# Kernel tuning notes

Hardware: AMD Instinct MI355X
Metric: run time of the kernel (lower is better)

## Reference

```python
import jax, jax.numpy as jnp
import numpy as np

B, S, H = 2, 1024, 1024
N_IN, N_PROC = 512, 32


def _l2norm(x, eps=1e-12):
    n = jnp.linalg.norm(x, axis=-1, keepdims=True)
    return x / jnp.maximum(n, eps)


def setup_inputs() -> dict:
    key = jax.random.key(0)
    k1, k2, k3, k4 = jax.random.split(key, 4)
    intermediate = jax.random.normal(k1, (B, S, H), dtype=jnp.float32)
    input_activations = jax.random.normal(k2, (B, S, N_IN), dtype=jnp.float32)
    # params (torch defaults: pattern_templates ~ randn; Linear weight ~ U scaled)
    pattern_templates = jax.random.normal(k3, (N_PROC, N_IN), dtype=jnp.float32)
    bound = 1.0 / np.sqrt(H)
    W_transform = jax.random.uniform(k4, (N_PROC * H, H), dtype=jnp.float32,
                                     minval=-bound, maxval=bound)
    return {"intermediate": intermediate, "input_activations": input_activations,
            "pattern_templates": pattern_templates, "W_transform": W_transform}


def reference(intermediate, input_activations, pattern_templates, W_transform):
    # pattern matching -> soft routing weights  [B,S,N_proc]
    act_norm = _l2norm(input_activations)
    tmpl_norm = _l2norm(pattern_templates)
    process_activations = jax.nn.sigmoid(
        jnp.einsum('bsi,ni->bsn', act_norm, tmpl_norm))
    # dispatch: weighted sum over sequence (batched GEMM instead of bcast-mul-sum)
    contexts = jnp.einsum('bsh,bsn->bnh', intermediate, process_activations)
    norm = process_activations.sum(axis=1)[..., None] + 1e-8  # [B,N_proc,1]
    contexts = contexts / norm
    # per-process-neuron HxH transform (torch Linear weight is [out,in])
    Wn = W_transform.reshape(N_PROC, H, H)  # [n, k(out), h(in)]
    transformed = jnp.einsum('bnh,nkh->bnk', contexts, Wn)
    # combine back to tokens  [B,S,H]
    combined = jnp.einsum('bnh,bsn->bsh', transformed, process_activations)
    return combined, process_activations
```

## Files before the change

kernel.cpp:

```cpp
#include <hip/hip_runtime.h>
#include <math.h>

#define B 2
#define S 1024
#define H 1024
#define NIN 512
#define NP 32
#define SC 16
#define SCHUNK (S / SC)

__global__ void k_pattern(const float* __restrict__ act, const float* __restrict__ tmpl,
                          float* __restrict__ P, float* __restrict__ nrm) {
    __shared__ float act_lds[8][NIN];
    __shared__ float invn[NP];
    __shared__ float psum[8][NP];
    int tid = threadIdx.x;
    int t0 = blockIdx.x * 8;
    int b  = t0 >> 10;

    {
        int n = tid >> 3, sub = tid & 7;
        const float* tr = tmpl + (size_t)n * NIN;
        float ss = 0.f;
#pragma unroll 16
        for (int k = 0; k < 64; ++k) { float x = tr[sub + 8 * k]; ss += x * x; }
        ss += __shfl_xor(ss, 1);
        ss += __shfl_xor(ss, 2);
        ss += __shfl_xor(ss, 4);
        if (sub == 0) invn[n] = 1.f / fmaxf(sqrtf(ss), 1e-12f);
    }
    {
        const float* src = act + (size_t)t0 * NIN;
        float* dst = &act_lds[0][0];
        for (int k = tid; k < 8 * NIN; k += 256) dst[k] = src[k];
    }
    __syncthreads();

    int tok = tid >> 5;
    int n   = tid & 31;
    float ss = 0.f;
#pragma unroll
    for (int k = 0; k < 16; ++k) { float x = act_lds[tok][n + 32 * k]; ss += x * x; }
#pragma unroll
    for (int m = 16; m; m >>= 1) ss += __shfl_xor(ss, m);
    float inva = 1.f / fmaxf(sqrtf(ss), 1e-12f);

    const float4* t4 = (const float4*)(tmpl + (size_t)n * NIN);
    const float4* a4 = (const float4*)(&act_lds[tok][0]);
    float d = 0.f;
#pragma unroll 8
    for (int i = 0; i < NIN / 4; ++i) {
        float4 tv = t4[i];
        float4 av = a4[i];
        d += tv.x * av.x + tv.y * av.y + tv.z * av.z + tv.w * av.w;
    }
    d *= inva * invn[n];
    float p = 1.f / (1.f + expf(-d));
    P[(size_t)(t0 + tok) * NP + n] = p;

    psum[tok][n] = p;
    __syncthreads();
    if (tid < NP) {
        float s = 0.f;
#pragma unroll
        for (int t = 0; t < 8; ++t) s += psum[t][tid];
        unsafeAtomicAdd(&nrm[b * NP + tid], s);
    }
}

__global__ void k_ctx(const float* __restrict__ I, const float* __restrict__ P,
                      float* __restrict__ ctx) {
    int bid = blockIdx.x;
    int ht = bid & 7;
    int sc = (bid >> 3) & (SC - 1);
    int b  = bid >> 7;
    int tid = threadIdx.x;
    __shared__ float Pl[SCHUNK][NP];
    int s0 = sc * SCHUNK;
    {
        const float* src = P + ((size_t)b * S + s0) * NP;
        float* dst = &Pl[0][0];
        for (int k = tid; k < SCHUNK * NP; k += 256) dst[k] = src[k];
    }
    __syncthreads();
    int hl = tid & 127;
    int g  = tid >> 7;
    int h  = ht * 128 + hl;
    float acc[16];
#pragma unroll
    for (int j = 0; j < 16; ++j) acc[j] = 0.f;
    const float* Ip = I + ((size_t)b * S + s0) * H + h;
    for (int s = 0; s < SCHUNK; ++s) {
        float x = Ip[(size_t)s * H];
#pragma unroll
        for (int j = 0; j < 16; ++j) acc[j] += x * Pl[s][g * 16 + j];
    }
#pragma unroll
    for (int j = 0; j < 16; ++j)
        unsafeAtomicAdd(&ctx[((size_t)b * NP + g * 16 + j) * H + h], acc[j]);
}

__global__ __launch_bounds__(256, 4)
void k_transform(const float* __restrict__ W, const float* __restrict__ ctx,
                 const float* __restrict__ nrm, float* __restrict__ T) {
    int bid = blockIdx.x;
    int n  = bid >> 6;
    int rg = bid & 63;
    int tid = threadIdx.x;
    int w = tid >> 6, lane = tid & 63;

    float inv0 = 1.f / (nrm[n] + 1e-8f);
    float inv1 = 1.f / (nrm[NP + n] + 1e-8f);

    const float4* c0g = (const float4*)(ctx + (size_t)n * H);
    const float4* c1g = (const float4*)(ctx + ((size_t)NP + n) * H);
    float4 c0[4], c1[4];
#pragma unroll
    for (int it = 0; it < 4; ++it) {
        float4 v = c0g[it * 64 + lane];
        c0[it] = make_float4(v.x * inv0, v.y * inv0, v.z * inv0, v.w * inv0);
        float4 u = c1g[it * 64 + lane];
        c1[it] = make_float4(u.x * inv1, u.y * inv1, u.z * inv1, u.w * inv1);
    }

    int row0 = rg * 16 + w * 4;
    const float4* Wr = (const float4*)(W + ((size_t)n * H + row0) * H);
    float a0[4] = {0.f, 0.f, 0.f, 0.f};
    float a1[4] = {0.f, 0.f, 0.f, 0.f};
#pragma unroll
    for (int it = 0; it < 4; ++it) {
#pragma unroll
        for (int r = 0; r < 4; ++r) {
            float4 wv = Wr[r * 256 + it * 64 + lane];
            a0[r] += wv.x * c0[it].x + wv.y * c0[it].y + wv.z * c0[it].z + wv.w * c0[it].w;
            a1[r] += wv.x * c1[it].x + wv.y * c1[it].y + wv.z * c1[it].z + wv.w * c1[it].w;
        }
    }
#pragma unroll
    for (int r = 0; r < 4; ++r) {
#pragma unroll
        for (int off = 32; off; off >>= 1) {
            a0[r] += __shfl_xor(a0[r], off);
            a1[r] += __shfl_xor(a1[r], off);
        }
    }
    if (lane == 0) {
#pragma unroll
        for (int r = 0; r < 4; ++r) {
            T[(size_t)n * H + row0 + r] = a0[r];
            T[((size_t)NP + n) * H + row0 + r] = a1[r];
        }
    }
}

__global__ void k_combine(const float* __restrict__ T, const float* __restrict__ P,
                          float* __restrict__ out) {
    int bid = blockIdx.x;
    int ht = bid & 3;
    int sc = (bid >> 2) & 63;
    int b  = bid >> 8;
    int tid = threadIdx.x;
    __shared__ float Tl[NP][256];
    __shared__ float Pl[16][NP];
    int h0 = ht * 256;
    for (int k = tid; k < NP * 256; k += 256) {
        int n = k >> 8, h = k & 255;
        Tl[n][h] = T[((size_t)b * NP + n) * H + h0 + h];
    }
    int s0 = sc * 16;
    {
        const float* src = P + ((size_t)b * S + s0) * NP;
        float* dst = &Pl[0][0];
        for (int k = tid; k < 16 * NP; k += 256) dst[k] = src[k];
    }
    __syncthreads();
    for (int s = 0; s < 16; ++s) {
        float acc = 0.f;
#pragma unroll
        for (int n = 0; n < NP; ++n) acc += Pl[s][n] * Tl[n][tid];
        out[((size_t)b * S + s0 + s) * H + h0 + tid] = acc;
    }
}

extern "C" void kernel_launch(void* const* d_in, const int* in_sizes, int n_in,
                              void* d_out, int out_size, void* d_ws, size_t ws_size,
                              hipStream_t stream) {
    const float* I    = (const float*)d_in[0];
    const float* act  = (const float*)d_in[1];
    const float* tmpl = (const float*)d_in[2];
    const float* W    = (const float*)d_in[3];
    float* out  = (float*)d_out;
    float* Pout = out + (size_t)B * S * H;

    float* ws  = (float*)d_ws;
    float* ctx = ws;
    float* nrm = ctx + (size_t)B * NP * H;
    float* T   = nrm + B * NP;

    hipMemsetAsync(ctx, 0, (size_t)(B * NP * H + B * NP) * sizeof(float), stream);
    k_pattern  <<<B * S / 8,              256, 0, stream>>>(act, tmpl, Pout, nrm);
    k_ctx      <<<B * SC * 8,             256, 0, stream>>>(I, Pout, ctx);
    k_transform<<<NP * 64,                256, 0, stream>>>(W, ctx, nrm, T);
    k_combine  <<<B * (S/16) * (H/256),   256, 0, stream>>>(T, Pout, out);
}
```

Measured before the change: 78.91 us.

## Restructure pattern dot, replace ctx atomics with partial+reduce, register-block combine

k_pattern now has each lane compute partial dots against all 32 templates over a slice of the activation, then reduces them with wave shuffles, so template reads are spread across lanes instead of each lane streaming one template row. k_ctx writes per-chunk partial sums to workspace, and a new reduce kernel sums them, which removes the float atomics and most of the memset at the cost of an extra launch and extra global traffic. k_combine keeps 16 output rows in registers and reads P directly from global memory instead of staging it in LDS. P is also read directly in ctx instead of through LDS.

```diff
diff --git a/kernel.cpp b/kernel.cpp
--- a/kernel.cpp
+++ b/kernel.cpp
@@ -9,8 +9,9 @@
 #define SC 16
 #define SCHUNK (S / SC)
 
-__global__ void k_pattern(const float* __restrict__ act, const float* __restrict__ tmpl,
-                          float* __restrict__ P, float* __restrict__ nrm) {
+__global__ __launch_bounds__(256)
+void k_pattern(const float* __restrict__ act, const float* __restrict__ tmpl,
+               float* __restrict__ P, float* __restrict__ nrm) {
     __shared__ float act_lds[8][NIN];
     __shared__ float invn[NP];
     __shared__ float psum[8][NP];
@@ -19,46 +20,58 @@
     int b  = t0 >> 10;
 
     {
-        int n = tid >> 3, sub = tid & 7;
+        const float4* src = (const float4*)(act + (size_t)t0 * NIN);
+        float4* dst = (float4*)(&act_lds[0][0]);
+        for (int k = tid; k < 8 * NIN / 4; k += 256) dst[k] = src[k];
+    }
+    {
+        int n = tid >> 3, s8 = tid & 7;
         const float* tr = tmpl + (size_t)n * NIN;
         float ss = 0.f;
 #pragma unroll 16
-        for (int k = 0; k < 64; ++k) { float x = tr[sub + 8 * k]; ss += x * x; }
-        ss += __shfl_xor(ss, 1);
-        ss += __shfl_xor(ss, 2);
-        ss += __shfl_xor(ss, 4);
-        if (sub == 0) invn[n] = 1.f / fmaxf(sqrtf(ss), 1e-12f);
-    }
-    {
-        const float* src = act + (size_t)t0 * NIN;
-        float* dst = &act_lds[0][0];
-        for (int k = tid; k < 8 * NIN; k += 256) dst[k] = src[k];
+        for (int k = 0; k < 64; ++k) { float x = tr[s8 + 8 * k]; ss += x * x; }
+        ss += __shfl_xor(ss, 1); ss += __shfl_xor(ss, 2); ss += __shfl_xor(ss, 4);
+        if (s8 == 0) invn[n] = 1.f / fmaxf(sqrtf(ss), 1e-12f);
     }
     __syncthreads();
 
     int tok = tid >> 5;
-    int n   = tid & 31;
+    int sub = tid & 31;
     float ss = 0.f;
 #pragma unroll
-    for (int k = 0; k < 16; ++k) { float x = act_lds[tok][n + 32 * k]; ss += x * x; }
+    for (int k = 0; k < 16; ++k) { float x = act_lds[tok][sub + 32 * k]; ss += x * x; }
 #pragma unroll
     for (int m = 16; m; m >>= 1) ss += __shfl_xor(ss, m);
     float inva = 1.f / fmaxf(sqrtf(ss), 1e-12f);
 
-    const float4* t4 = (const float4*)(tmpl + (size_t)n * NIN);
-    const float4* a4 = (const float4*)(&act_lds[tok][0]);
-    float d = 0.f;
-#pragma unroll 8
-    for (int i = 0; i < NIN / 4; ++i) {
-        float4 tv = t4[i];
-        float4 av = a4[i];
-        d += tv.x * av.x + tv.y * av.y + tv.z * av.z + tv.w * av.w;
-    }
-    d *= inva * invn[n];
-    float p = 1.f / (1.f + expf(-d));
-    P[(size_t)(t0 + tok) * NP + n] = p;
-
-    psum[tok][n] = p;
+    float4 av[4];
+#pragma unroll
+    for (int q = 0; q < 4; ++q)
+        av[q] = *(const float4*)(&act_lds[tok][sub * 4 + q * 128]);
+
+    float dot[NP];
+#pragma unroll
+    for (int n = 0; n < NP; ++n) {
+        const float* tr = tmpl + (size_t)n * NIN + sub * 4;
+        float d = 0.f;
+#pragma unroll
+        for (int q = 0; q < 4; ++q) {
+            float4 tv = *(const float4*)(tr + q * 128);
+            d += tv.x * av[q].x + tv.y * av[q].y + tv.z * av[q].z + tv.w * av[q].w;
+        }
+        dot[n] = d;
+    }
+    float myd = 0.f;
+#pragma unroll
+    for (int n = 0; n < NP; ++n) {
+        float d = dot[n];
+        d += __shfl_xor(d, 1); d += __shfl_xor(d, 2); d += __shfl_xor(d, 4);
+        d += __shfl_xor(d, 8); d += __shfl_xor(d, 16);
+        if (sub == n) myd = d;
+    }
+    float p = 1.f / (1.f + expf(-myd * inva * invn[sub]));
+    P[(size_t)(t0 + tok) * NP + sub] = p;
+    psum[tok][sub] = p;
     __syncthreads();
     if (tid < NP) {
         float s = 0.f;
@@ -68,36 +81,44 @@
     }
 }
 
-__global__ void k_ctx(const float* __restrict__ I, const float* __restrict__ P,
-                      float* __restrict__ ctx) {
+__global__ __launch_bounds__(256)
+void k_ctx_partial(const float* __restrict__ I, const float* __restrict__ P,
+                   float* __restrict__ part) {
     int bid = blockIdx.x;
     int ht = bid & 7;
     int sc = (bid >> 3) & (SC - 1);
     int b  = bid >> 7;
     int tid = threadIdx.x;
-    __shared__ float Pl[SCHUNK][NP];
+    int hl = tid & 127;
+    int g  = __builtin_amdgcn_readfirstlane(tid >> 7);
+    int h  = ht * 128 + hl;
     int s0 = sc * SCHUNK;
-    {
-        const float* src = P + ((size_t)b * S + s0) * NP;
-        float* dst = &Pl[0][0];
-        for (int k = tid; k < SCHUNK * NP; k += 256) dst[k] = src[k];
-    }
-    __syncthreads();
-    int hl = tid & 127;
-    int g  = tid >> 7;
-    int h  = ht * 128 + hl;
+    const float* Pb = P + ((size_t)b * S + s0) * NP + g * 16;
+    const float* Ip = I + ((size_t)b * S + s0) * H + h;
     float acc[16];
 #pragma unroll
     for (int j = 0; j < 16; ++j) acc[j] = 0.f;
-    const float* Ip = I + ((size_t)b * S + s0) * H + h;
+#pragma unroll 4
     for (int s = 0; s < SCHUNK; ++s) {
         float x = Ip[(size_t)s * H];
 #pragma unroll
-        for (int j = 0; j < 16; ++j) acc[j] += x * Pl[s][g * 16 + j];
-    }
-#pragma unroll
-    for (int j = 0; j < 16; ++j)
-        unsafeAtomicAdd(&ctx[((size_t)b * NP + g * 16 + j) * H + h], acc[j]);
+        for (int j = 0; j < 16; ++j) acc[j] += x * Pb[s * NP + j];
+    }
+    size_t base = (((size_t)b * SC + sc) * NP + g * 16) * H + h;
+#pragma unroll
+    for (int j = 0; j < 16; ++j) part[base + (size_t)j * H] = acc[j];
+}
+
+__global__ __launch_bounds__(256)
+void k_ctx_reduce(const float* __restrict__ part, float* __restrict__ ctx) {
+    int idx = blockIdx.x * 256 + threadIdx.x;
+    int b = idx >> 15;
+    int rem = idx & 32767;
+    float s = 0.f;
+#pragma unroll
+    for (int sc = 0; sc < SC; ++sc)
+        s += part[((size_t)b * SC + sc) * (NP * H) + rem];
+    ctx[idx] = s;
 }
 
 __global__ __launch_bounds__(256, 4)
@@ -153,33 +174,41 @@
     }
 }
 
-__global__ void k_combine(const float* __restrict__ T, const float* __restrict__ P,
-                          float* __restrict__ out) {
+__global__ __launch_bounds__(256)
+void k_combine(const float* __restrict__ T, const float* __restrict__ P,
+               float* __restrict__ out) {
     int bid = blockIdx.x;
     int ht = bid & 3;
     int sc = (bid >> 2) & 63;
     int b  = bid >> 8;
     int tid = threadIdx.x;
     __shared__ float Tl[NP][256];
-    __shared__ float Pl[16][NP];
     int h0 = ht * 256;
     for (int k = tid; k < NP * 256; k += 256) {
         int n = k >> 8, h = k & 255;
         Tl[n][h] = T[((size_t)b * NP + n) * H + h0 + h];
     }
+    __syncthreads();
     int s0 = sc * 16;
-    {
-        const float* src = P + ((size_t)b * S + s0) * NP;
-        float* dst = &Pl[0][0];
-        for (int k = tid; k < 16 * NP; k += 256) dst[k] = src[k];
-    }
-    __syncthreads();
-    for (int s = 0; s < 16; ++s) {
-        float acc = 0.f;
-#pragma unroll
-        for (int n = 0; n < NP; ++n) acc += Pl[s][n] * Tl[n][tid];
-        out[((size_t)b * S + s0 + s) * H + h0 + tid] = acc;
-    }
+    const float* Pb = P + ((size_t)b * S + s0) * NP;
+    float acc[16];
+#pragma unroll
+    for (int s = 0; s < 16; ++s) acc[s] = 0.f;
+#pragma unroll
+    for (int n0 = 0; n0 < NP; n0 += 4) {
+        float t0v = Tl[n0 + 0][tid];
+        float t1v = Tl[n0 + 1][tid];
+        float t2v = Tl[n0 + 2][tid];
+        float t3v = Tl[n0 + 3][tid];
+#pragma unroll
+        for (int s = 0; s < 16; ++s) {
+            const float* pr = Pb + s * NP + n0;
+            acc[s] += t0v * pr[0] + t1v * pr[1] + t2v * pr[2] + t3v * pr[3];
+        }
+    }
+#pragma unroll
+    for (int s = 0; s < 16; ++s)
+        out[((size_t)b * S + s0 + s) * H + h0 + tid] = acc[s];
 }
 
 extern "C" void kernel_launch(void* const* d_in, const int* in_sizes, int n_in,
@@ -192,14 +221,16 @@
     float* out  = (float*)d_out;
     float* Pout = out + (size_t)B * S * H;
 
-    float* ws  = (float*)d_ws;
-    float* ctx = ws;
-    float* nrm = ctx + (size_t)B * NP * H;
-    float* T   = nrm + B * NP;
-
-    hipMemsetAsync(ctx, 0, (size_t)(B * NP * H + B * NP) * sizeof(float), stream);
-    k_pattern  <<<B * S / 8,              256, 0, stream>>>(act, tmpl, Pout, nrm);
-    k_ctx      <<<B * SC * 8,             256, 0, stream>>>(I, Pout, ctx);
-    k_transform<<<NP * 64,                256, 0, stream>>>(W, ctx, nrm, T);
-    k_combine  <<<B * (S/16) * (H/256),   256, 0, stream>>>(T, Pout, out);
-}
+    float* ws   = (float*)d_ws;
+    float* nrm  = ws;
+    float* part = nrm + 64;
+    float* ctx  = part + (size_t)B * SC * NP * H;
+    float* T    = ctx + (size_t)B * NP * H;
+
+    hipMemsetAsync(nrm, 0, (size_t)B * NP * sizeof(float), stream);
+    k_pattern    <<<B * S / 8,            256, 0, stream>>>(act, tmpl, Pout, nrm);
+    k_ctx_partial<<<B * SC * 8,           256, 0, stream>>>(I, Pout, part);
+    k_ctx_reduce <<<B * NP * H / 256,     256, 0, stream>>>(part, ctx);
+    k_transform  <<<NP * 64,              256, 0, stream>>>(W, ctx, nrm, T);
+    k_combine    <<<B * 64 * 4,           256, 0, stream>>>(T, Pout, out);
+}
```

Result: slower. 81.37 us (+3.1%).
